# Performance work log

Measured on AMD Instinct MI355X. Metric: run time of the kernel, lower is better.

Reference implementation:

```python
import jax, jax.numpy as jnp
import numpy as np

REPR_OUT = (16, 16, 16)   # multiplicities for l=0,1,2
STRIDE = 2                # GatedBlock stride with smooth_stride=True -> low-pass+stride after gate
PAD = 2                   # conv padding
C_IN = 72                 # 8*1 + 8*3 + 8*5
C_OUT_GATED = 176         # 144 fields + 32 gate scalars
KSIZE = 5


def conv3d(x, w, stride, padding):
    return jax.lax.conv_general_dilated(
        x, w, window_strides=(stride,) * 3,
        padding=[(padding, padding)] * 3,
        dimension_numbers=('NCDHW', 'OIDHW', 'NCDHW'))


def low_pass_filter(z, scale, stride):
    # gaussian blur (sigma from scale) applied depthwise, then strided -- as in se3cnn
    sigma = 0.5 * (scale ** 2 - 1) ** 0.5
    size = int(1 + 2 * 2.5 * sigma)
    if size % 2 == 0:
        size += 1
    r = np.arange(size) - size // 2
    g1 = np.exp(-r.astype(np.float64) ** 2 / (2 * sigma ** 2))
    g = g1[:, None, None] * g1[None, :, None] * g1[None, None, :]
    g = (g / g.sum()).astype(np.float32)
    B, C = z.shape[0], z.shape[1]
    zz = z.reshape(B * C, 1, *z.shape[2:])
    out = conv3d(zz, jnp.asarray(g)[None, None], stride, size // 2)
    return out.reshape(B, C, *out.shape[2:])


def gate(y, scalar_bias, gate_bias):
    # y: [B, 176, X, Y, Z]; split into 144 field channels + 32 gate scalars
    size_out = sum(mul * (2 * n + 1) for n, mul in enumerate(REPR_OUT))
    B, _, nx, ny, nz = y.shape
    g = jax.nn.sigmoid(y[:, size_out:] + gate_bias[None, :, None, None, None])
    fields = []
    begin_y, begin_g = 0, 0
    for n, mul in enumerate(REPR_OUT):
        if mul == 0:
            continue
        dim = 2 * n + 1
        fy = y[:, begin_y:begin_y + mul * dim]
        if n == 0:
            # scalar fields: bias + relu (ScalarActivation)
            fields.append(jax.nn.relu(fy + scalar_bias[None, :, None, None, None]))
        else:
            fg = g[:, begin_g:begin_g + mul]
            begin_g += mul
            f = fy.reshape(B, mul, dim, nx, ny, nz) * fg[:, :, None]  # broadcast gate over 2l+1
            fields.append(f.reshape(B, mul * dim, nx, ny, nz))
        begin_y += mul * dim
    return jnp.concatenate(fields, axis=1)  # [B, 144, X, Y, Z]


def setup_inputs() -> dict:
    key = jax.random.key(0)
    k1, k2, k3, k4 = jax.random.split(key, 4)
    fan_in = C_IN * KSIZE ** 3
    x = jax.random.normal(k1, (4, C_IN, 32, 32, 32), dtype=jnp.float32)
    W = jax.random.normal(k2, (C_OUT_GATED, C_IN, KSIZE, KSIZE, KSIZE), dtype=jnp.float32) / np.sqrt(fan_in)
    scalar_bias = jax.random.normal(k3, (REPR_OUT[0],), dtype=jnp.float32) * 0.1
    gate_bias = jax.random.normal(k4, (sum(REPR_OUT[1:]),), dtype=jnp.float32) * 0.1
    return {'x': x, 'W': W, 'scalar_bias': scalar_bias, 'gate_bias': gate_bias}


def reference(x, W, scalar_bias, gate_bias):
    y = conv3d(x, W, 1, PAD)                 # SE3 conv at stride 1 (smooth_stride)
    z = gate(y, scalar_bias, gate_bias)      # per-irrep gated nonlinearity
    z = low_pass_filter(z, STRIDE, STRIDE)   # gaussian low-pass + stride 2
    return z
```

## Files before the change

kernel.cpp:

```cpp
#include <hip/hip_runtime.h>
#include <cstdint>
#include <cstddef>

typedef short short8 __attribute__((ext_vector_type(8)));
typedef float floatx4 __attribute__((ext_vector_type(4)));
typedef unsigned short u16;

__device__ __forceinline__ u16 f2bf(float f) {
    unsigned u = __float_as_uint(f);
    u += 0x7FFFu + ((u >> 16) & 1u);
    return (u16)(u >> 16);
}
__device__ __forceinline__ float bf2f(u16 h) {
    return __uint_as_float(((unsigned)h) << 16);
}

__device__ __forceinline__ void gload_lds16(const u16* g, u16* l) {
    __builtin_amdgcn_global_load_lds(
        (const __attribute__((address_space(1))) void*)g,
        (__attribute__((address_space(3))) void*)l, 16, 0, 0);
}

__global__ __launch_bounds__(256) void k_transpose_x(const float* __restrict__ x,
                                                     u16* __restrict__ xt) {
    __shared__ float tile[72 * 33];
    const int bx = blockIdx.x;
    const int tid = threadIdx.x;
    const int b = bx >> 10, d = (bx >> 5) & 31, h = bx & 31;
    const float* src = x + (size_t)b * 72 * 32768 + d * 1024 + h * 32;
    for (int e = tid; e < 2304; e += 256) {
        int ci = e >> 5, w = e & 31;
        tile[ci * 33 + w] = src[(size_t)ci * 32768 + w];
    }
    __syncthreads();
    u16* dst = xt + (size_t)bx * 2304;
    for (int e = tid; e < 2304; e += 256) {
        int w = e / 72, ci = e - w * 72;
        dst[e] = f2bf(tile[ci * 33 + w]);
    }
}

__global__ __launch_bounds__(256) void k_prep_w(const float* __restrict__ W,
                                                u16* __restrict__ wt) {
    const int gid = blockIdx.x * 256 + threadIdx.x;
    const int frag = gid >> 6, lane = gid & 63;
    const int nb = frag % 11;
    int t = frag / 11;
    const int kb = t % 12;
    t = t / 12;
    const int kh = t % 5, kd = t / 5;
    const int n = lane & 15, q8 = (lane >> 4) * 8;
    const int co = nb * 16 + n;
    u16 v[8] __attribute__((aligned(16)));
    #pragma unroll
    for (int j = 0; j < 8; ++j) {
        int k = kb * 32 + q8 + j;
        u16 r = 0;
        if (k < 360) {
            int kw = k / 72, ci = k - kw * 72;
            r = f2bf(W[((size_t)co * 72 + ci) * 125 + kd * 25 + kh * 5 + kw]);
        }
        v[j] = r;
    }
    *(uint4*)(wt + (size_t)gid * 8) = *(const uint4*)v;
}

#define LP 2624

#define CONV_STEP(kb_, bufc_, bufn_) do {                                          \
    const int kkn_ = kh * 12 + (kb_) + 1;                                          \
    if (kkn_ < 60) {              \
        const u16* gsrc_ = wt_kd + (size_t)kkn_ * 5632;                            \
        gload_lds16(gsrc_ + wv * 512 + lane * 8, sB + (bufn_) * 5632 + wv * 512);  \
        if (wv < 3)                                                                \
            gload_lds16(gsrc_ + (8 + wv) * 512 + lane * 8,                         \
                        sB + (bufn_) * 5632 + (8 + wv) * 512);                     \
    }                                                                              \
    const u16* ap_ = sxrow + (kb_) * 32;                                           \
    short8 A0_ = *(const short8*)(ap_);                                            \
    short8 A1_ = *(const short8*)(ap_ + 1152);                                     \
    short8 A2_ = *(const short8*)(ap_ + LP);                                       \
    short8 A3_ = *(const short8*)(ap_ + LP + 1152);                                \
    const u16* bb_ = sB + (bufc_) * 5632 + lane * 8;                               \
    _Pragma("unroll")                                                              \
    for (int nb = 0; nb < 11; ++nb) {                                              \
        short8 bv = *(const short8*)(bb_ + nb * 512);                              \
        acc[0][nb] = __builtin_amdgcn_mfma_f32_16x16x32_bf16(A0_, bv, acc[0][nb], 0, 0, 0); \
        acc[1][nb] = __builtin_amdgcn_mfma_f32_16x16x32_bf16(A1_, bv, acc[1][nb], 0, 0, 0); \
        acc[2][nb] = __builtin_amdgcn_mfma_f32_16x16x32_bf16(A2_, bv, acc[2][nb], 0, 0, 0); \
        acc[3][nb] = __builtin_amdgcn_mfma_f32_16x16x32_bf16(A3_, bv, acc[3][nb], 0, 0, 0); \
    }                                                                              \
    __syncthreads();                                                               \
} while (0)

__global__ __launch_bounds__(512, 2) void k_conv(const u16* __restrict__ xt,
                                                 const u16* __restrict__ wt,
                                                 const float* __restrict__ scalar_bias,
                                                 const float* __restrict__ gate_bias,
                                                 u16* __restrict__ zt) {
    __shared__ __align__(16) u16 sx[20 * LP];
    __shared__ __align__(16) u16 sB[2 * 5632];
    const int bx = blockIdx.x;
    const int ht = bx & 1, d = (bx >> 1) & 31, b = bx >> 6;
    const int h0 = ht * 16;
    const int tid = threadIdx.x, lane = tid & 63, wv = tid >> 6;
    const int c15 = lane & 15, q = lane >> 4;

    floatx4 acc[4][11];
    #pragma unroll
    for (int i = 0; i < 4; ++i) {
        #pragma unroll
        for (int j = 0; j < 11; ++j) acc[i][j] = (floatx4){0.f, 0.f, 0.f, 0.f};
    }

    const int laneA = c15 * 72 + q * 8;

    for (int kd = 0; kd < 5; ++kd) {
        const int dp = d + kd - 2;
        if (dp < 0 || dp >= 32) continue;
        const u16* srcbase = xt + (size_t)((b * 32 + dp) * 32) * 2304;
        for (int idx = tid; idx < 20 * 328; idx += 512) {
            int r = idx / 328, c = idx - r * 328;
            int hp = h0 + r - 2;
            uint4 val = make_uint4(0u, 0u, 0u, 0u);
            if (hp >= 0 && hp < 32 && c >= 18 && c < 306)
                val = *(const uint4*)(srcbase + (size_t)hp * 2304 + (c * 8 - 144));
            *(uint4*)(&sx[r * LP + c * 8]) = val;
        }
        const u16* wt_kd = wt + (size_t)kd * 5 * 67584;
        gload_lds16(wt_kd + wv * 512 + lane * 8, sB + wv * 512);
        if (wv < 3)
            gload_lds16(wt_kd + (8 + wv) * 512 + lane * 8, sB + (8 + wv) * 512);
        __syncthreads();

        for (int kh = 0; kh < 5; ++kh) {
            const u16* sxrow = &sx[(2 * wv + kh) * LP + laneA];
            #pragma unroll 1
            for (int kbp = 0; kbp < 6; ++kbp) {
                CONV_STEP(2 * kbp,     0, 1);
                CONV_STEP(2 * kbp + 1, 1, 0);
            }
        }
    }

    const float sb = scalar_bias[c15];
    int   slA[9];
    float gbA[9];
    #pragma unroll
    for (int nb = 1; nb <= 8; ++nb) {
        int idx = (nb - 1) * 16 + c15;
        int mul = (nb <= 3) ? (idx / 3) : (16 + (idx - 48) / 5);
        slA[nb] = (lane & 48) | (mul & 15);
        gbA[nb] = gate_bias[mul];
    }
    #pragma unroll
    for (int mi = 0; mi < 4; ++mi) {
        const int hl = 2 * wv + (mi >> 1);
        const int wh = mi & 1;
        const size_t zrow0 = (size_t)((b * 32 + d) * 32 + (h0 + hl)) * 32;
        #pragma unroll
        for (int r = 0; r < 4; ++r) {
            const int w = wh * 16 + q * 4 + r;
            u16* zp = zt + (zrow0 + w) * 144;
            zp[c15] = f2bf(fmaxf(acc[mi][0][r] + sb, 0.f));
            const float g9v  = acc[mi][9][r];
            const float g10v = acc[mi][10][r];
            #pragma unroll
            for (int nb = 1; nb <= 8; ++nb) {
                float ys = __shfl((nb <= 3) ? g9v : g10v, slA[nb], 64);
                float g  = 1.f / (1.f + __expf(-(ys + gbA[nb])));
                zp[nb * 16 + c15] = f2bf(acc[mi][nb][r] * g);
            }
        }
    }
}

__global__ __launch_bounds__(256) void k_lowpass(const u16* __restrict__ zt,
                                                 float* __restrict__ out) {
    const int gid = blockIdx.x * 256 + threadIdx.x;
    const int row = gid / 288;
    const int it  = gid - row * 288;
    const int c8 = it >> 4, ow = it & 15;
    const int oh = row & 15, od = (row >> 4) & 15, b = row >> 8;
    const float lw[5] = {0.03208210f, 0.23705644f, 0.46172277f, 0.23705644f, 0.03208210f};
    float a[8];
    #pragma unroll
    for (int j = 0; j < 8; ++j) a[j] = 0.f;
    for (int kd = 0; kd < 5; ++kd) {
        const int dz = 2 * od + kd - 2;
        if (dz < 0 || dz >= 32) continue;
        for (int kh = 0; kh < 5; ++kh) {
            const int hz = 2 * oh + kh - 2;
            if (hz < 0 || hz >= 32) continue;
            const float whd = lw[kd] * lw[kh];
            const u16* base = zt + (size_t)((b * 32 + dz) * 32 + hz) * 32 * 144 + c8 * 8;
            #pragma unroll
            for (int kw = 0; kw < 5; ++kw) {
                const int wz = 2 * ow + kw - 2;
                if (wz < 0 || wz >= 32) continue;
                const float wt3 = whd * lw[kw];
                u16 v[8] __attribute__((aligned(16)));
                *(uint4*)v = *(const uint4*)(base + (size_t)wz * 144);
                #pragma unroll
                for (int j = 0; j < 8; ++j) a[j] += wt3 * bf2f(v[j]);
            }
        }
    }
    const int c0 = c8 * 8;
    float* op = out + ((size_t)b * 144 + c0) * 4096 + od * 256 + oh * 16 + ow;
    #pragma unroll
    for (int j = 0; j < 8; ++j) op[(size_t)j * 4096] = a[j];
}

extern "C" void kernel_launch(void* const* d_in, const int* in_sizes, int n_in,
                              void* d_out, int out_size, void* d_ws, size_t ws_size,
                              hipStream_t stream) {
    const float* x  = (const float*)d_in[0];
    const float* W  = (const float*)d_in[1];
    const float* sb = (const float*)d_in[2];
    const float* gb = (const float*)d_in[3];
    float* out = (float*)d_out;

    char* ws = (char*)d_ws;
    u16* xt = (u16*)(ws);
    u16* wt = (u16*)(ws + 18874368);
    u16* zt = (u16*)(ws + 22253568);

    hipLaunchKernelGGL(k_transpose_x, dim3(4096), dim3(256), 0, stream, x, xt);
    hipLaunchKernelGGL(k_prep_w,      dim3(825),  dim3(256), 0, stream, W, wt);
    hipLaunchKernelGGL(k_conv,        dim3(256),  dim3(512), 0, stream, xt, wt, sb, gb, zt);
    hipLaunchKernelGGL(k_lowpass,     dim3(1152), dim3(256), 0, stream, zt, out);
}
```

Measured before the change: 510.8 us.

## Load conv weight fragments directly into registers with triple-buffered prefetch, drop LDS staging

Weight (B) fragments are no longer staged through a double-buffered LDS tile with global_load_lds and a __syncthreads every k-step. Each wave now loads its 11 B fragments straight from global/L2 into registers, rotating three register buffers so the prefetch runs two steps ahead. This removes the per-step block barriers and LDS traffic for weights. In exchange every wave issues redundant global loads of the same weights, and 33 short8 registers on top of 44 accumulators raise register pressure under launch_bounds(512,2), risking spills.

```diff
diff --git a/kernel.cpp b/kernel.cpp
--- a/kernel.cpp
+++ b/kernel.cpp
@@ -13,12 +13,6 @@
 }
 __device__ __forceinline__ float bf2f(u16 h) {
     return __uint_as_float(((unsigned)h) << 16);
-}
-
-__device__ __forceinline__ void gload_lds16(const u16* g, u16* l) {
-    __builtin_amdgcn_global_load_lds(
-        (const __attribute__((address_space(1))) void*)g,
-        (__attribute__((address_space(3))) void*)l, 16, 0, 0);
 }
 
 __global__ __launch_bounds__(256) void k_transpose_x(const float* __restrict__ x,
@@ -67,30 +61,27 @@
 
 #define LP 2624
 
-#define CONV_STEP(kb_, bufc_, bufn_) do {                                          \
-    const int kkn_ = kh * 12 + (kb_) + 1;                                          \
-    if (kkn_ < 60) {              \
-        const u16* gsrc_ = wt_kd + (size_t)kkn_ * 5632;                            \
-        gload_lds16(gsrc_ + wv * 512 + lane * 8, sB + (bufn_) * 5632 + wv * 512);  \
-        if (wv < 3)                                                                \
-            gload_lds16(gsrc_ + (8 + wv) * 512 + lane * 8,                         \
-                        sB + (bufn_) * 5632 + (8 + wv) * 512);                     \
-    }                                                                              \
-    const u16* ap_ = sxrow + (kb_) * 32;                                           \
+#define MFMA_BF16 __builtin_amdgcn_mfma_f32_16x16x32_bf16
+
+#define STEP(Bc, Bn, kkc) do {                                                     \
+    const int kh_ = (kkc) / 12;                                                    \
+    const int kb_ = (kkc) - 12 * kh_;                                              \
+    const u16* ap_ = sxA + kh_ * LP + kb_ * 32;                                    \
     short8 A0_ = *(const short8*)(ap_);                                            \
     short8 A1_ = *(const short8*)(ap_ + 1152);                                     \
     short8 A2_ = *(const short8*)(ap_ + LP);                                       \
     short8 A3_ = *(const short8*)(ap_ + LP + 1152);                                \
-    const u16* bb_ = sB + (bufc_) * 5632 + lane * 8;                               \
+    const int kkn_ = ((kkc) + 2 < 60) ? ((kkc) + 2) : 59;                          \
+    const u16* gp_ = wt_kd + (size_t)kkn_ * 5632 + lane * 8;                       \
     _Pragma("unroll")                                                              \
-    for (int nb = 0; nb < 11; ++nb) {                                              \
-        short8 bv = *(const short8*)(bb_ + nb * 512);                              \
-        acc[0][nb] = __builtin_amdgcn_mfma_f32_16x16x32_bf16(A0_, bv, acc[0][nb], 0, 0, 0); \
-        acc[1][nb] = __builtin_amdgcn_mfma_f32_16x16x32_bf16(A1_, bv, acc[1][nb], 0, 0, 0); \
-        acc[2][nb] = __builtin_amdgcn_mfma_f32_16x16x32_bf16(A2_, bv, acc[2][nb], 0, 0, 0); \
-        acc[3][nb] = __builtin_amdgcn_mfma_f32_16x16x32_bf16(A3_, bv, acc[3][nb], 0, 0, 0); \
+    for (int j = 0; j < 11; ++j) Bn[j] = *(const short8*)(gp_ + j * 512);          \
+    _Pragma("unroll")                                                              \
+    for (int j = 0; j < 11; ++j) {                                                 \
+        acc[0][j] = MFMA_BF16(A0_, Bc[j], acc[0][j], 0, 0, 0);                     \
+        acc[1][j] = MFMA_BF16(A1_, Bc[j], acc[1][j], 0, 0, 0);                     \
+        acc[2][j] = MFMA_BF16(A2_, Bc[j], acc[2][j], 0, 0, 0);                     \
+        acc[3][j] = MFMA_BF16(A3_, Bc[j], acc[3][j], 0, 0, 0);                     \
     }                                                                              \
-    __syncthreads();                                                               \
 } while (0)
 
 __global__ __launch_bounds__(512, 2) void k_conv(const u16* __restrict__ xt,
@@ -99,7 +90,6 @@
                                                  const float* __restrict__ gate_bias,
                                                  u16* __restrict__ zt) {
     __shared__ __align__(16) u16 sx[20 * LP];
-    __shared__ __align__(16) u16 sB[2 * 5632];
     const int bx = blockIdx.x;
     const int ht = bx & 1, d = (bx >> 1) & 31, b = bx >> 6;
     const int h0 = ht * 16;
@@ -114,11 +104,15 @@
     }
 
     const int laneA = c15 * 72 + q * 8;
+    const u16* sxA = &sx[2 * wv * LP + laneA];
+
+    short8 B0[11], B1[11], B2[11];
 
     for (int kd = 0; kd < 5; ++kd) {
         const int dp = d + kd - 2;
         if (dp < 0 || dp >= 32) continue;
         const u16* srcbase = xt + (size_t)((b * 32 + dp) * 32) * 2304;
+        __syncthreads();
         for (int idx = tid; idx < 20 * 328; idx += 512) {
             int r = idx / 328, c = idx - r * 328;
             int hp = h0 + r - 2;
@@ -128,18 +122,21 @@
             *(uint4*)(&sx[r * LP + c * 8]) = val;
         }
         const u16* wt_kd = wt + (size_t)kd * 5 * 67584;
-        gload_lds16(wt_kd + wv * 512 + lane * 8, sB + wv * 512);
-        if (wv < 3)
-            gload_lds16(wt_kd + (8 + wv) * 512 + lane * 8, sB + (8 + wv) * 512);
+        {
+            const u16* g0 = wt_kd + lane * 8;
+            #pragma unroll
+            for (int j = 0; j < 11; ++j) B0[j] = *(const short8*)(g0 + j * 512);
+            const u16* g1 = wt_kd + 5632 + lane * 8;
+            #pragma unroll
+            for (int j = 0; j < 11; ++j) B1[j] = *(const short8*)(g1 + j * 512);
+        }
         __syncthreads();
 
-        for (int kh = 0; kh < 5; ++kh) {
-            const u16* sxrow = &sx[(2 * wv + kh) * LP + laneA];
-            #pragma unroll 1
-            for (int kbp = 0; kbp < 6; ++kbp) {
-                CONV_STEP(2 * kbp,     0, 1);
-                CONV_STEP(2 * kbp + 1, 1, 0);
-            }
+        #pragma unroll 1
+        for (int kk = 0; kk < 60; kk += 3) {
+            STEP(B0, B2, kk);
+            STEP(B1, B0, kk + 1);
+            STEP(B2, B1, kk + 2);
         }
     }
 
```

New measurement: 1.295 ms. 153% more time.
